# Kernel optimization log

Hardware: AMD Instinct MI355X
Metric: run time of the kernel (lower is better)

The kernel has to match this reference:

```python
import jax, jax.numpy as jnp
import numpy as np

B, S, IN_DIM, D_MODEL, H = 1, 4096, 512, 512, 8
DK = D_MODEL // H


def setup_inputs() -> dict:
    key = jax.random.key(0)
    ks = jax.random.split(key, 10)
    sc_in = 1.0 / np.sqrt(IN_DIM)
    sc_dm = 1.0 / np.sqrt(D_MODEL)
    return {
        "x": jax.random.normal(ks[0], (B, S, IN_DIM), dtype=jnp.float32),
        "mask": jax.random.randint(ks[1], (1, 1, S, S), 0, 2, dtype=jnp.int32),
        "wq_w": jax.random.uniform(ks[2], (D_MODEL, IN_DIM), jnp.float32, -sc_in, sc_in),
        "wq_b": jax.random.uniform(ks[3], (D_MODEL,), jnp.float32, -sc_in, sc_in),
        "wk_w": jax.random.uniform(ks[4], (D_MODEL, IN_DIM), jnp.float32, -sc_in, sc_in),
        "wk_b": jax.random.uniform(ks[5], (D_MODEL,), jnp.float32, -sc_in, sc_in),
        "wv_w": jax.random.uniform(ks[6], (D_MODEL, IN_DIM), jnp.float32, -sc_in, sc_in),
        "wv_b": jax.random.uniform(ks[7], (D_MODEL,), jnp.float32, -sc_in, sc_in),
        "dense_w": jax.random.uniform(ks[8], (D_MODEL, D_MODEL), jnp.float32, -sc_dm, sc_dm),
        "dense_b": jax.random.uniform(ks[9], (D_MODEL,), jnp.float32, -sc_dm, sc_dm),
    }


def _split_heads(t):
    # Faithful to original: raw view [B, S, D] -> [B, H, S, DK] (no transpose)
    return t.reshape(B, H, S, DK)


def reference(x, mask, wq_w, wq_b, wk_w, wk_b, wv_w, wv_b, dense_w, dense_b):
    q = _split_heads(x @ wq_w.T + wq_b)  # [B, H, S, DK]
    k = _split_heads(x @ wk_w.T + wk_b)
    v = _split_heads(x @ wv_w.T + wv_b)
    score = jnp.einsum("bhqd,bhkd->bhqk", q, k) / np.sqrt(DK).astype(np.float32)
    score = score + mask.astype(score.dtype) * (-1e9)
    attn = jax.nn.softmax(score, axis=-1)
    out = jnp.einsum("bhqk,bhkd->bhqd", attn, v)  # [B, H, S, DK]
    out = out.transpose(0, 2, 1, 3).reshape(B, S, D_MODEL)
    return out @ dense_w.T + dense_b
```

## Files before the change

kernel.cpp:

```cpp
#include <hip/hip_runtime.h>
#include <hip/hip_bf16.h>

#define S_LEN 4096
#define DM    512
#define NH    8
#define DK    64

typedef __attribute__((ext_vector_type(8))) __bf16 bf16x8;
typedef __attribute__((ext_vector_type(4))) float  f32x4;
typedef unsigned short u16;
typedef unsigned int   u32;
typedef unsigned long long u64;

#define SQ_SCALE (0.125f * 1.44269504f)
#define FMAX 12.0f

#define NPART 8
#define KSPAN 512

__device__ __forceinline__ u16 f2bf(float f) {
  union { float f; u32 i; } v; v.f = f;
  u32 r = v.i + 0x7fff + ((v.i >> 16) & 1);
  return (u16)(r >> 16);
}
__device__ __forceinline__ float bf2f(u16 u) {
  union { u32 i; float f; } v; v.i = ((u32)u) << 16; return v.f;
}

__global__ __launch_bounds__(256) void pack_mask(const int* __restrict__ mask,
                                                 u64* __restrict__ out) {
  int gid = blockIdx.x * 256 + threadIdx.x;
  u64 b = __ballot(mask[gid] != 0);
  if ((threadIdx.x & 63) == 0) out[gid >> 6] = b;
}

__global__ __launch_bounds__(256) void convert_all(
    const float* __restrict__ x, const float* __restrict__ wq,
    const float* __restrict__ wk, const float* __restrict__ wv,
    const float* __restrict__ dw,
    u16* __restrict__ xb, u16* __restrict__ wcat, u16* __restrict__ dwb) {
  int b = blockIdx.x;
  const float* src; u16* dst; size_t off;
  if      (b < 2048) { src = x;  dst = xb;   off = (size_t)b * 1024; }
  else if (b < 2304) { src = wq; dst = wcat; off = (size_t)(b - 2048) * 1024; }
  else if (b < 2560) { src = wk; dst = wcat + 262144; off = (size_t)(b - 2304) * 1024; }
  else if (b < 2816) { src = wv; dst = wcat + 524288; off = (size_t)(b - 2560) * 1024; }
  else               { src = dw; dst = dwb;  off = (size_t)(b - 2816) * 1024; }
  size_t i = off + (size_t)threadIdx.x * 4;
  float4 v = *reinterpret_cast<const float4*>(src + i);
  ushort4 o = make_ushort4(f2bf(v.x), f2bf(v.y), f2bf(v.z), f2bf(v.w));
  *reinterpret_cast<ushort4*>(dst + i) = o;
}

__global__ __launch_bounds__(256) void qkv_gemm(
    const u16* __restrict__ A, const u16* __restrict__ Wcat,
    const float* __restrict__ bq, const float* __restrict__ bk,
    const float* __restrict__ bv,
    u16* __restrict__ Qb, u16* __restrict__ Kb, u16* __restrict__ V4) {
  __shared__ u16 As[64 * 72];
  __shared__ u16 Ws[128 * 72];
  const int t = threadIdx.x;
  const int lane = t & 63, wv = t >> 6;
  const int m16 = lane & 15, quad = lane >> 4;
  const int n0g = blockIdx.x * 128, m0 = blockIdx.y * 64;
  const int seg = n0g >> 9;
  const int n0 = n0g & 511;
  const int mq = wv >> 1, nq = wv & 1;

  f32x4 acc[2][4];
#pragma unroll
  for (int i = 0; i < 2; i++)
#pragma unroll
    for (int j = 0; j < 4; j++) acc[i][j] = (f32x4)0.f;

  for (int k0 = 0; k0 < DM; k0 += 64) {
    __syncthreads();
#pragma unroll
    for (int c0 = 0; c0 < 2; c0++) {
      int c = t + c0 * 256;
      int row = c >> 3, col = (c & 7) * 8;
      *reinterpret_cast<uint4*>(&As[row * 72 + col]) =
          *reinterpret_cast<const uint4*>(&A[(size_t)(m0 + row) * DM + k0 + col]);
    }
#pragma unroll
    for (int c0 = 0; c0 < 4; c0++) {
      int c = t + c0 * 256;
      int row = c >> 3, col = (c & 7) * 8;
      *reinterpret_cast<uint4*>(&Ws[row * 72 + col]) =
          *reinterpret_cast<const uint4*>(&Wcat[(size_t)(n0g + row) * DM + k0 + col]);
    }
    __syncthreads();
#pragma unroll
    for (int kk = 0; kk < 64; kk += 32) {
      bf16x8 a0 = *reinterpret_cast<const bf16x8*>(&As[(mq * 32 + m16) * 72 + quad * 8 + kk]);
      bf16x8 a1 = *reinterpret_cast<const bf16x8*>(&As[(mq * 32 + 16 + m16) * 72 + quad * 8 + kk]);
#pragma unroll
      for (int ct = 0; ct < 4; ct++) {
        bf16x8 b = *reinterpret_cast<const bf16x8*>(&Ws[(nq * 64 + ct * 16 + m16) * 72 + quad * 8 + kk]);
        acc[0][ct] = __builtin_amdgcn_mfma_f32_16x16x32_bf16(a0, b, acc[0][ct], 0, 0, 0);
        acc[1][ct] = __builtin_amdgcn_mfma_f32_16x16x32_bf16(a1, b, acc[1][ct], 0, 0, 0);
      }
    }
  }

  const float* bias = (seg == 0) ? bq : (seg == 1) ? bk : bv;
  const float scale = (seg == 0) ? SQ_SCALE : 1.f;
  float bn[4];
#pragma unroll
  for (int ct = 0; ct < 4; ct++) bn[ct] = bias[n0 + nq * 64 + ct * 16 + m16];

  if (seg == 2) {
    __syncthreads();
    u16* T = Ws;
#pragma unroll
    for (int rt = 0; rt < 2; rt++)
#pragma unroll
      for (int ct = 0; ct < 4; ct++)
#pragma unroll
        for (int r = 0; r < 4; r++)
          T[(nq * 64 + ct * 16 + m16) * 72 + mq * 32 + rt * 16 + quad * 4 + r] =
              f2bf(acc[rt][ct][r] + bn[ct]);
    __syncthreads();
    const int h    = m0 >> 9;
    const int mp   = m0 & 511;
    const int cseg = n0 >> 7;
#pragma unroll
    for (int c0 = 0; c0 < 4; c0++) {
      int c = t + c0 * 256;
      int d  = c >> 4;
      int tl = (c >> 1) & 7;
      int cl = c & 1;
      uint4 v = *reinterpret_cast<const uint4*>(&T[(cl * 64 + d) * 72 + tl * 8]);
      *reinterpret_cast<uint4*>(
          &V4[(size_t)(h * 64 + d) * 4096 + ((mp >> 3) + tl) * 64 + cl * 32 + cseg * 8]) = v;
    }
  } else {
    u16* dst = (seg == 0) ? Qb : Kb;
#pragma unroll
    for (int rt = 0; rt < 2; rt++)
#pragma unroll
      for (int ct = 0; ct < 4; ct++) {
        int n = n0 + nq * 64 + ct * 16 + m16;
#pragma unroll
        for (int r = 0; r < 4; r++) {
          int m = m0 + mq * 32 + rt * 16 + quad * 4 + r;
          dst[(size_t)m * DM + n] = f2bf((acc[rt][ct][r] + bn[ct]) * scale);
        }
      }
  }
}

__global__ __launch_bounds__(256) void dense_gemm(
    const u16* __restrict__ A, const u16* __restrict__ W,
    const float* __restrict__ bias, float* __restrict__ Cout) {
  __shared__ u16 As[64 * 72];
  __shared__ u16 Ws[64 * 72];
  const int t = threadIdx.x;
  const int lane = t & 63, wv = t >> 6;
  const int m16 = lane & 15, quad = lane >> 4;
  const int n0 = blockIdx.x * 64, m0 = blockIdx.y * 64;

  f32x4 acc[4];
#pragma unroll
  for (int j = 0; j < 4; j++) acc[j] = (f32x4)0.f;

  for (int k0 = 0; k0 < DM; k0 += 64) {
    __syncthreads();
#pragma unroll
    for (int c0 = 0; c0 < 2; c0++) {
      int c = t + c0 * 256;
      int row = c >> 3, col = (c & 7) * 8;
      *reinterpret_cast<uint4*>(&As[row * 72 + col]) =
          *reinterpret_cast<const uint4*>(&A[(size_t)(m0 + row) * DM + k0 + col]);
      *reinterpret_cast<uint4*>(&Ws[row * 72 + col]) =
          *reinterpret_cast<const uint4*>(&W[(size_t)(n0 + row) * DM + k0 + col]);
    }
    __syncthreads();
#pragma unroll
    for (int kk = 0; kk < 64; kk += 32) {
      bf16x8 a = *reinterpret_cast<const bf16x8*>(&As[(wv * 16 + m16) * 72 + quad * 8 + kk]);
#pragma unroll
      for (int ct = 0; ct < 4; ct++) {
        bf16x8 b = *reinterpret_cast<const bf16x8*>(&Ws[(ct * 16 + m16) * 72 + quad * 8 + kk]);
        acc[ct] = __builtin_amdgcn_mfma_f32_16x16x32_bf16(a, b, acc[ct], 0, 0, 0);
      }
    }
  }

  float bn[4];
#pragma unroll
  for (int ct = 0; ct < 4; ct++) bn[ct] = bias[n0 + ct * 16 + m16];
#pragma unroll
  for (int ct = 0; ct < 4; ct++) {
    int n = n0 + ct * 16 + m16;
#pragma unroll
    for (int r = 0; r < 4; r++) {
      int m = m0 + wv * 16 + quad * 4 + r;
      Cout[(size_t)m * DM + n] = acc[ct][r] + bn[ct];
    }
  }
}

__device__ __forceinline__ void pack_p(const f32x4* s, u32 lo, u32 hi,
                                       uint4& o0, uint4& o1) {
  u32 pk[8];
#pragma unroll
  for (int ct = 0; ct < 4; ct++) {
    u32 w = (ct & 1) ? hi : lo;
    int b = ct >> 1;
    float p0 = __builtin_amdgcn_exp2f(((w >> b) & 1u)        ? -1e9f : s[ct][0]);
    float p1 = __builtin_amdgcn_exp2f(((w >> (b + 8)) & 1u)  ? -1e9f : s[ct][1]);
    float p2 = __builtin_amdgcn_exp2f(((w >> (b + 16)) & 1u) ? -1e9f : s[ct][2]);
    float p3 = __builtin_amdgcn_exp2f(((w >> (b + 24)) & 1u) ? -1e9f : s[ct][3]);
    pk[2 * ct]     = __builtin_amdgcn_perm(__float_as_uint(p1) + 0x8000u,
                                           __float_as_uint(p0) + 0x8000u, 0x07060302u);
    pk[2 * ct + 1] = __builtin_amdgcn_perm(__float_as_uint(p3) + 0x8000u,
                                           __float_as_uint(p2) + 0x8000u, 0x07060302u);
  }
  o0 = make_uint4(pk[0], pk[1], pk[2], pk[3]);
  o1 = make_uint4(pk[4], pk[5], pk[6], pk[7]);
}

__global__ __launch_bounds__(256, 4) void attn_mfma(
    const u16* __restrict__ Q, const u16* __restrict__ K,
    const u16* __restrict__ V4, const u64* __restrict__ mbits,
    u16* __restrict__ Op, float* __restrict__ Lp) {
  __shared__ u16 Ks[64 * 72];
  __shared__ u16 Vs[64 * 72];

  const int t = threadIdx.x;
  const int lane = t & 63, w4 = t >> 6;
  const int m16 = lane & 15, quad = lane >> 4;
  const int q0 = blockIdx.x * 128;
  const int h = blockIdx.y;
  const int g = blockIdx.z;
  const size_t hoff = (size_t)h * S_LEN * DK;
  const size_t kbase = hoff + (size_t)g * KSPAN * DK;

  const u16* qpA = Q + hoff + (size_t)(q0 + w4 * 32 + m16) * DK + quad * 8;
  bf16x8 qloA = *reinterpret_cast<const bf16x8*>(qpA);
  bf16x8 qhiA = *reinterpret_cast<const bf16x8*>(qpA + 32);
  bf16x8 qloB = *reinterpret_cast<const bf16x8*>(qpA + 16 * DK);
  bf16x8 qhiB = *reinterpret_cast<const bf16x8*>(qpA + 16 * DK + 32);

  union { u16 u[8]; bf16x8 v; } onesu;
#pragma unroll
  for (int j = 0; j < 8; j++) onesu.u[j] = 0x3F80;
  const bf16x8 ones = onesu.v;

  f32x4 accA[4], accB[4];
  f32x4 acc_lA = (f32x4)0.f, acc_lB = (f32x4)0.f;
#pragma unroll
  for (int dt = 0; dt < 4; dt++) { accA[dt] = (f32x4)0.f; accB[dt] = (f32x4)0.f; }

  for (int k0 = 0; k0 < KSPAN; k0 += 64) {
    const int kg = g * KSPAN + k0;
#pragma unroll
    for (int c0 = 0; c0 < 2; c0++) {
      int c = t + c0 * 256;
      int rg = c >> 3, cc = c & 7;
      int sr = ((rg & 1) << 5) | (((rg >> 5) & 1) << 4) | (((rg >> 2) & 1) << 3) |
               (((rg >> 1) & 1) << 2) | (((rg >> 4) & 1) << 1) | ((rg >> 3) & 1);
      *reinterpret_cast<uint4*>(&Ks[sr * 72 + cc * 8]) =
          *reinterpret_cast<const uint4*>(&K[kbase + (size_t)(k0 + rg) * DK + cc * 8]);
      *reinterpret_cast<uint4*>(&Vs[rg * 72 + cc * 8]) =
          *reinterpret_cast<const uint4*>(&V4[(size_t)(h * 64 + rg) * 4096 + kg + cc * 8]);
    }
    u64 mqA = mbits[(size_t)(q0 + w4 * 32 + m16) * 64 + (kg >> 6)] >> (2 * quad);
    u64 mqB = mbits[(size_t)(q0 + w4 * 32 + 16 + m16) * 64 + (kg >> 6)] >> (2 * quad);
    __syncthreads();

    f32x4 sA[4], sB[4];
#pragma unroll
    for (int ct = 0; ct < 4; ct++) { sA[ct] = (f32x4)(-FMAX); sB[ct] = (f32x4)(-FMAX); }
#pragma unroll
    for (int ct = 0; ct < 4; ct++) {
      bf16x8 klo = *reinterpret_cast<const bf16x8*>(&Ks[(ct * 16 + m16) * 72 + quad * 8]);
      bf16x8 khi = *reinterpret_cast<const bf16x8*>(&Ks[(ct * 16 + m16) * 72 + quad * 8 + 32]);
      sA[ct] = __builtin_amdgcn_mfma_f32_16x16x32_bf16(klo, qloA, sA[ct], 0, 0, 0);
      sA[ct] = __builtin_amdgcn_mfma_f32_16x16x32_bf16(khi, qhiA, sA[ct], 0, 0, 0);
      sB[ct] = __builtin_amdgcn_mfma_f32_16x16x32_bf16(klo, qloB, sB[ct], 0, 0, 0);
      sB[ct] = __builtin_amdgcn_mfma_f32_16x16x32_bf16(khi, qhiB, sB[ct], 0, 0, 0);
    }

    union { uint4 i; bf16x8 v; } pA0, pA1, pB0, pB1;
    pack_p(sA, (u32)mqA, (u32)(mqA >> 32), pA0.i, pA1.i);
    pack_p(sB, (u32)mqB, (u32)(mqB >> 32), pB0.i, pB1.i);

#pragma unroll
    for (int dt = 0; dt < 4; dt++) {
      bf16x8 vlo = *reinterpret_cast<const bf16x8*>(&Vs[(dt * 16 + m16) * 72 + quad * 8]);
      bf16x8 vhi = *reinterpret_cast<const bf16x8*>(&Vs[(dt * 16 + m16) * 72 + quad * 8 + 32]);
      accA[dt] = __builtin_amdgcn_mfma_f32_16x16x32_bf16(pA0.v, vlo, accA[dt], 0, 0, 0);
      accA[dt] = __builtin_amdgcn_mfma_f32_16x16x32_bf16(pA1.v, vhi, accA[dt], 0, 0, 0);
      accB[dt] = __builtin_amdgcn_mfma_f32_16x16x32_bf16(pB0.v, vlo, accB[dt], 0, 0, 0);
      accB[dt] = __builtin_amdgcn_mfma_f32_16x16x32_bf16(pB1.v, vhi, accB[dt], 0, 0, 0);
    }
    acc_lA = __builtin_amdgcn_mfma_f32_16x16x32_bf16(pA0.v, ones, acc_lA, 0, 0, 0);
    acc_lA = __builtin_amdgcn_mfma_f32_16x16x32_bf16(pA1.v, ones, acc_lA, 0, 0, 0);
    acc_lB = __builtin_amdgcn_mfma_f32_16x16x32_bf16(pB0.v, ones, acc_lB, 0, 0, 0);
    acc_lB = __builtin_amdgcn_mfma_f32_16x16x32_bf16(pB1.v, ones, acc_lB, 0, 0, 0);
    __syncthreads();
  }

  u16* Og = Op + (size_t)g * 2097152;
#pragma unroll
  for (int dt = 0; dt < 4; dt++)
#pragma unroll
    for (int r = 0; r < 4; r++) {
      Og[(size_t)(q0 + w4 * 32 + quad * 4 + r) * DM + h * DK + dt * 16 + m16] =
          f2bf(accA[dt][r]);
      Og[(size_t)(q0 + w4 * 32 + 16 + quad * 4 + r) * DM + h * DK + dt * 16 + m16] =
          f2bf(accB[dt][r]);
    }
  if (m16 == 0) {
#pragma unroll
    for (int r = 0; r < 4; r++) {
      Lp[g * 32768 + h * 4096 + q0 + w4 * 32 + quad * 4 + r] = acc_lA[r];
      Lp[g * 32768 + h * 4096 + q0 + w4 * 32 + 16 + quad * 4 + r] = acc_lB[r];
    }
  }
}

__global__ __launch_bounds__(256) void attn_merge(
    const u16* __restrict__ Op, const float* __restrict__ Lp,
    u16* __restrict__ Out) {
  int i8 = (blockIdx.x * 256 + threadIdx.x) * 8;
  int q = i8 >> 9;
  int h = (i8 >> 6) & 7;
  float l = 0.f;
#pragma unroll
  for (int part = 0; part < NPART; part++) l += Lp[part * 32768 + h * 4096 + q];
  float rl = 1.f / l;
  float o[8];
#pragma unroll
  for (int j = 0; j < 8; j++) o[j] = 0.f;
#pragma unroll
  for (int part = 0; part < NPART; part++) {
    ushort4 v0 = *reinterpret_cast<const ushort4*>(Op + (size_t)part * 2097152 + i8);
    ushort4 v1 = *reinterpret_cast<const ushort4*>(Op + (size_t)part * 2097152 + i8 + 4);
    o[0] += bf2f(v0.x); o[1] += bf2f(v0.y); o[2] += bf2f(v0.z); o[3] += bf2f(v0.w);
    o[4] += bf2f(v1.x); o[5] += bf2f(v1.y); o[6] += bf2f(v1.z); o[7] += bf2f(v1.w);
  }
  ushort4 o0 = make_ushort4(f2bf(o[0] * rl), f2bf(o[1] * rl),
                            f2bf(o[2] * rl), f2bf(o[3] * rl));
  ushort4 o1 = make_ushort4(f2bf(o[4] * rl), f2bf(o[5] * rl),
                            f2bf(o[6] * rl), f2bf(o[7] * rl));
  *reinterpret_cast<ushort4*>(Out + i8) = o0;
  *reinterpret_cast<ushort4*>(Out + i8 + 4) = o1;
}

extern "C" void kernel_launch(void* const* d_in, const int* in_sizes, int n_in,
                              void* d_out, int out_size, void* d_ws, size_t ws_size,
                              hipStream_t stream) {
  const float* x    = (const float*)d_in[0];
  const int*   mask = (const int*)d_in[1];
  const float* wq_w = (const float*)d_in[2];
  const float* wq_b = (const float*)d_in[3];
  const float* wk_w = (const float*)d_in[4];
  const float* wk_b = (const float*)d_in[5];
  const float* wv_w = (const float*)d_in[6];
  const float* wv_b = (const float*)d_in[7];
  const float* dw   = (const float*)d_in[8];
  const float* db   = (const float*)d_in[9];

  u16* xb    = (u16*)d_ws;
  u16* wcat  = xb    + 2097152;
  u16* dwb   = wcat  + 786432;
  u16* Qb    = dwb   + 262144;
  u16* Kb    = Qb    + 2097152;
  u16* V4    = Kb    + 2097152;
  u16* Opart = V4    + 2097152;
  u64* mb    = (u64*)(Opart + (size_t)NPART * 2097152);
  float* Lp  = (float*)(mb + 262144);

  pack_mask<<<(S_LEN * S_LEN) / 256, 256, 0, stream>>>(mask, mb);
  convert_all<<<3072, 256, 0, stream>>>(x, wq_w, wk_w, wv_w, dw, xb, wcat, dwb);

  qkv_gemm<<<dim3(12, 64), 256, 0, stream>>>(xb, wcat, wq_b, wk_b, wv_b,
                                             Qb, Kb, V4);

  attn_mfma<<<dim3(32, NH, NPART), 256, 0, stream>>>(Qb, Kb, V4, mb, Opart, Lp);
  attn_merge<<<1024, 256, 0, stream>>>(Opart, Lp, Qb);

  dense_gemm<<<dim3(8, 64), 256, 0, stream>>>(Qb, dwb, db, (float*)d_out);
}
```

Before: 233.8 us.

## Register-prefetch next K/V tile, fold mask into accumulator init, halve key partitions

The attention loop now loads the next 64-key K/V tile and mask words into registers while the current tile is computed, then stores them to LDS at the top of the next iteration. This hides global-load latency behind the MFMA work. The mask is applied by initialising the score accumulators to -1e9 or -FMAX before the QK MFMAs, which removes the per-element selects from the exp packing. The key span per block doubles and the partition count halves, so there are fewer blocks and less partial-result combining, but each block runs longer and grid parallelism drops.

```diff
diff --git a/kernel.cpp b/kernel.cpp
--- a/kernel.cpp
+++ b/kernel.cpp
@@ -15,8 +15,8 @@
 #define SQ_SCALE (0.125f * 1.44269504f)
 #define FMAX 12.0f
 
-#define NPART 8
-#define KSPAN 512
+#define NPART 4
+#define KSPAN 1024
 
 __device__ __forceinline__ u16 f2bf(float f) {
   union { float f; u32 i; } v; v.f = f;
@@ -201,17 +201,14 @@
   }
 }
 
-__device__ __forceinline__ void pack_p(const f32x4* s, u32 lo, u32 hi,
-                                       uint4& o0, uint4& o1) {
+__device__ __forceinline__ void pack_p(const f32x4* s, uint4& o0, uint4& o1) {
   u32 pk[8];
 #pragma unroll
   for (int ct = 0; ct < 4; ct++) {
-    u32 w = (ct & 1) ? hi : lo;
-    int b = ct >> 1;
-    float p0 = __builtin_amdgcn_exp2f(((w >> b) & 1u)        ? -1e9f : s[ct][0]);
-    float p1 = __builtin_amdgcn_exp2f(((w >> (b + 8)) & 1u)  ? -1e9f : s[ct][1]);
-    float p2 = __builtin_amdgcn_exp2f(((w >> (b + 16)) & 1u) ? -1e9f : s[ct][2]);
-    float p3 = __builtin_amdgcn_exp2f(((w >> (b + 24)) & 1u) ? -1e9f : s[ct][3]);
+    float p0 = __builtin_amdgcn_exp2f(s[ct][0]);
+    float p1 = __builtin_amdgcn_exp2f(s[ct][1]);
+    float p2 = __builtin_amdgcn_exp2f(s[ct][2]);
+    float p3 = __builtin_amdgcn_exp2f(s[ct][3]);
     pk[2 * ct]     = __builtin_amdgcn_perm(__float_as_uint(p1) + 0x8000u,
                                            __float_as_uint(p0) + 0x8000u, 0x07060302u);
     pk[2 * ct + 1] = __builtin_amdgcn_perm(__float_as_uint(p3) + 0x8000u,
@@ -248,31 +245,65 @@
   for (int j = 0; j < 8; j++) onesu.u[j] = 0x3F80;
   const bf16x8 ones = onesu.v;
 
+  const int rg0 = t >> 3,          cc = t & 7;
+  const int rg1 = (t + 256) >> 3;
+  auto sigma = [](int rg) {
+    return ((rg & 1) << 5) | (((rg >> 5) & 1) << 4) | (((rg >> 2) & 1) << 3) |
+           (((rg >> 1) & 1) << 2) | (((rg >> 4) & 1) << 1) | ((rg >> 3) & 1);
+  };
+  const int sr0 = sigma(rg0), sr1 = sigma(rg1);
+  const u16* kp0 = &K[kbase + (size_t)rg0 * DK + cc * 8];
+  const u16* kp1 = &K[kbase + (size_t)rg1 * DK + cc * 8];
+  const u16* vp0 = &V4[(size_t)(h * 64 + rg0) * 4096 + g * KSPAN + cc * 8];
+  const u16* vp1 = &V4[(size_t)(h * 64 + rg1) * 4096 + g * KSPAN + cc * 8];
+  const u64* mpA = &mbits[(size_t)(q0 + w4 * 32 + m16) * 64 + ((g * KSPAN) >> 6)];
+  const u64* mpB = mpA + (size_t)16 * 64;
+
+  uint4 rk0 = *reinterpret_cast<const uint4*>(kp0);
+  uint4 rk1 = *reinterpret_cast<const uint4*>(kp1);
+  uint4 rv0 = *reinterpret_cast<const uint4*>(vp0);
+  uint4 rv1 = *reinterpret_cast<const uint4*>(vp1);
+  u64 rmA = *mpA, rmB = *mpB;
+
   f32x4 accA[4], accB[4];
   f32x4 acc_lA = (f32x4)0.f, acc_lB = (f32x4)0.f;
 #pragma unroll
   for (int dt = 0; dt < 4; dt++) { accA[dt] = (f32x4)0.f; accB[dt] = (f32x4)0.f; }
 
   for (int k0 = 0; k0 < KSPAN; k0 += 64) {
-    const int kg = g * KSPAN + k0;
-#pragma unroll
-    for (int c0 = 0; c0 < 2; c0++) {
-      int c = t + c0 * 256;
-      int rg = c >> 3, cc = c & 7;
-      int sr = ((rg & 1) << 5) | (((rg >> 5) & 1) << 4) | (((rg >> 2) & 1) << 3) |
-               (((rg >> 1) & 1) << 2) | (((rg >> 4) & 1) << 1) | ((rg >> 3) & 1);
-      *reinterpret_cast<uint4*>(&Ks[sr * 72 + cc * 8]) =
-          *reinterpret_cast<const uint4*>(&K[kbase + (size_t)(k0 + rg) * DK + cc * 8]);
-      *reinterpret_cast<uint4*>(&Vs[rg * 72 + cc * 8]) =
-          *reinterpret_cast<const uint4*>(&V4[(size_t)(h * 64 + rg) * 4096 + kg + cc * 8]);
-    }
-    u64 mqA = mbits[(size_t)(q0 + w4 * 32 + m16) * 64 + (kg >> 6)] >> (2 * quad);
-    u64 mqB = mbits[(size_t)(q0 + w4 * 32 + 16 + m16) * 64 + (kg >> 6)] >> (2 * quad);
+    __syncthreads();
+    *reinterpret_cast<uint4*>(&Ks[sr0 * 72 + cc * 8]) = rk0;
+    *reinterpret_cast<uint4*>(&Ks[sr1 * 72 + cc * 8]) = rk1;
+    *reinterpret_cast<uint4*>(&Vs[rg0 * 72 + cc * 8]) = rv0;
+    *reinterpret_cast<uint4*>(&Vs[rg1 * 72 + cc * 8]) = rv1;
+    u64 mA = rmA >> (2 * quad);
+    u64 mB = rmB >> (2 * quad);
+    if (k0 + 64 < KSPAN) {
+      kp0 += 64 * DK; kp1 += 64 * DK; vp0 += 64; vp1 += 64;
+      rk0 = *reinterpret_cast<const uint4*>(kp0);
+      rk1 = *reinterpret_cast<const uint4*>(kp1);
+      rv0 = *reinterpret_cast<const uint4*>(vp0);
+      rv1 = *reinterpret_cast<const uint4*>(vp1);
+      rmA = mpA[(k0 >> 6) + 1];
+      rmB = mpB[(k0 >> 6) + 1];
+    }
     __syncthreads();
 
     f32x4 sA[4], sB[4];
-#pragma unroll
-    for (int ct = 0; ct < 4; ct++) { sA[ct] = (f32x4)(-FMAX); sB[ct] = (f32x4)(-FMAX); }
+    u32 loA = (u32)mA, hiA = (u32)(mA >> 32);
+    u32 loB = (u32)mB, hiB = (u32)(mB >> 32);
+#pragma unroll
+    for (int ct = 0; ct < 4; ct++) {
+      u32 wA = (ct & 1) ? hiA : loA;
+      u32 wB = (ct & 1) ? hiB : loB;
+      int b = ct >> 1;
+#pragma unroll
+      for (int r = 0; r < 4; r++) {
+        sA[ct][r] = ((wA >> (b + 8 * r)) & 1u) ? -1e9f : -FMAX;
+        sB[ct][r] = ((wB >> (b + 8 * r)) & 1u) ? -1e9f : -FMAX;
+      }
+    }
+
 #pragma unroll
     for (int ct = 0; ct < 4; ct++) {
       bf16x8 klo = *reinterpret_cast<const bf16x8*>(&Ks[(ct * 16 + m16) * 72 + quad * 8]);
@@ -284,8 +315,8 @@
     }
 
     union { uint4 i; bf16x8 v; } pA0, pA1, pB0, pB1;
-    pack_p(sA, (u32)mqA, (u32)(mqA >> 32), pA0.i, pA1.i);
-    pack_p(sB, (u32)mqB, (u32)(mqB >> 32), pB0.i, pB1.i);
+    pack_p(sA, pA0.i, pA1.i);
+    pack_p(sB, pB0.i, pB1.i);
 
 #pragma unroll
     for (int dt = 0; dt < 4; dt++) {
@@ -300,7 +331,6 @@
     acc_lA = __builtin_amdgcn_mfma_f32_16x16x32_bf16(pA1.v, ones, acc_lA, 0, 0, 0);
     acc_lB = __builtin_amdgcn_mfma_f32_16x16x32_bf16(pB0.v, ones, acc_lB, 0, 0, 0);
     acc_lB = __builtin_amdgcn_mfma_f32_16x16x32_bf16(pB1.v, ones, acc_lB, 0, 0, 0);
-    __syncthreads();
   }
 
   u16* Og = Op + (size_t)g * 2097152;
```

Result: slower. 252.2 us (+7.9%).

## Load K/V fragments directly from global memory, drop LDS and barriers, remap grid

Applied to the files above, without the earlier changes.

The attention kernel no longer stages K and V tiles through shared memory with __syncthreads; each lane reads its MFMA operand fragments straight from global memory, with the K row permutation folded into precomputed per-lane pointers. The split-K factor goes from 8 partitions of 512 keys to 4 partitions of 1024, and the grid is flattened to 1024 blocks with a custom index mapping so that the blocks sharing a q-tile land near each other. This removes LDS traffic and barrier stalls, but the four waves in a block each reload the same K/V data from L1/L2 and get fewer but longer blocks. The merge kernel still launches 1024 blocks over partials, so it relies on the unseen merge code using NPART.

```diff
diff --git a/kernel.cpp b/kernel.cpp
--- a/kernel.cpp
+++ b/kernel.cpp
@@ -15,8 +15,8 @@
 #define SQ_SCALE (0.125f * 1.44269504f)
 #define FMAX 12.0f
 
-#define NPART 8
-#define KSPAN 512
+#define NPART 4
+#define KSPAN 1024
 
 __device__ __forceinline__ u16 f2bf(float f) {
   union { float f; u32 i; } v; v.f = f;
@@ -225,15 +225,14 @@
     const u16* __restrict__ Q, const u16* __restrict__ K,
     const u16* __restrict__ V4, const u64* __restrict__ mbits,
     u16* __restrict__ Op, float* __restrict__ Lp) {
-  __shared__ u16 Ks[64 * 72];
-  __shared__ u16 Vs[64 * 72];
-
   const int t = threadIdx.x;
   const int lane = t & 63, w4 = t >> 6;
   const int m16 = lane & 15, quad = lane >> 4;
-  const int q0 = blockIdx.x * 128;
-  const int h = blockIdx.y;
-  const int g = blockIdx.z;
+  const int lin = blockIdx.x;
+  const int q0 = ((lin >> 3) & 31) * 128;
+  const int hg = ((lin >> 8) << 3) | (lin & 7);
+  const int h = hg & 7;
+  const int g = hg >> 3;
   const size_t hoff = (size_t)h * S_LEN * DK;
   const size_t kbase = hoff + (size_t)g * KSPAN * DK;
 
@@ -243,6 +242,14 @@
   bf16x8 qloB = *reinterpret_cast<const bf16x8*>(qpA + 16 * DK);
   bf16x8 qhiB = *reinterpret_cast<const bf16x8*>(qpA + 16 * DK + 32);
 
+  const u16* kct[4];
+#pragma unroll
+  for (int ct = 0; ct < 4; ct++) {
+    int row = ((ct & 1) << 5) | (((m16 >> 1) & 1) << 4) | ((m16 & 1) << 3) |
+              (((m16 >> 3) & 1) << 2) | (((m16 >> 2) & 1) << 1) | (ct >> 1);
+    kct[ct] = K + kbase + (size_t)row * DK + quad * 8;
+  }
+
   union { u16 u[8]; bf16x8 v; } onesu;
 #pragma unroll
   for (int j = 0; j < 8; j++) onesu.u[j] = 0x3F80;
@@ -253,30 +260,23 @@
 #pragma unroll
   for (int dt = 0; dt < 4; dt++) { accA[dt] = (f32x4)0.f; accB[dt] = (f32x4)0.f; }
 
+  const u16* vt0 = V4 + (size_t)(h * 64 + m16) * 4096 + g * KSPAN + quad * 8;
+  const u64* mpA = &mbits[(size_t)(q0 + w4 * 32 + m16) * 64 + ((g * KSPAN) >> 6)];
+  const u64* mpB = mpA + (size_t)16 * 64;
+
+#pragma unroll 1
   for (int k0 = 0; k0 < KSPAN; k0 += 64) {
-    const int kg = g * KSPAN + k0;
-#pragma unroll
-    for (int c0 = 0; c0 < 2; c0++) {
-      int c = t + c0 * 256;
-      int rg = c >> 3, cc = c & 7;
-      int sr = ((rg & 1) << 5) | (((rg >> 5) & 1) << 4) | (((rg >> 2) & 1) << 3) |
-               (((rg >> 1) & 1) << 2) | (((rg >> 4) & 1) << 1) | ((rg >> 3) & 1);
-      *reinterpret_cast<uint4*>(&Ks[sr * 72 + cc * 8]) =
-          *reinterpret_cast<const uint4*>(&K[kbase + (size_t)(k0 + rg) * DK + cc * 8]);
-      *reinterpret_cast<uint4*>(&Vs[rg * 72 + cc * 8]) =
-          *reinterpret_cast<const uint4*>(&V4[(size_t)(h * 64 + rg) * 4096 + kg + cc * 8]);
-    }
-    u64 mqA = mbits[(size_t)(q0 + w4 * 32 + m16) * 64 + (kg >> 6)] >> (2 * quad);
-    u64 mqB = mbits[(size_t)(q0 + w4 * 32 + 16 + m16) * 64 + (kg >> 6)] >> (2 * quad);
-    __syncthreads();
+    u64 mqA = mpA[k0 >> 6] >> (2 * quad);
+    u64 mqB = mpB[k0 >> 6] >> (2 * quad);
 
     f32x4 sA[4], sB[4];
 #pragma unroll
     for (int ct = 0; ct < 4; ct++) { sA[ct] = (f32x4)(-FMAX); sB[ct] = (f32x4)(-FMAX); }
+    const size_t koff = (size_t)k0 * DK;
 #pragma unroll
     for (int ct = 0; ct < 4; ct++) {
-      bf16x8 klo = *reinterpret_cast<const bf16x8*>(&Ks[(ct * 16 + m16) * 72 + quad * 8]);
-      bf16x8 khi = *reinterpret_cast<const bf16x8*>(&Ks[(ct * 16 + m16) * 72 + quad * 8 + 32]);
+      bf16x8 klo = *reinterpret_cast<const bf16x8*>(kct[ct] + koff);
+      bf16x8 khi = *reinterpret_cast<const bf16x8*>(kct[ct] + koff + 32);
       sA[ct] = __builtin_amdgcn_mfma_f32_16x16x32_bf16(klo, qloA, sA[ct], 0, 0, 0);
       sA[ct] = __builtin_amdgcn_mfma_f32_16x16x32_bf16(khi, qhiA, sA[ct], 0, 0, 0);
       sB[ct] = __builtin_amdgcn_mfma_f32_16x16x32_bf16(klo, qloB, sB[ct], 0, 0, 0);
@@ -287,10 +287,11 @@
     pack_p(sA, (u32)mqA, (u32)(mqA >> 32), pA0.i, pA1.i);
     pack_p(sB, (u32)mqB, (u32)(mqB >> 32), pB0.i, pB1.i);
 
+    const u16* vt = vt0 + k0;
 #pragma unroll
     for (int dt = 0; dt < 4; dt++) {
-      bf16x8 vlo = *reinterpret_cast<const bf16x8*>(&Vs[(dt * 16 + m16) * 72 + quad * 8]);
-      bf16x8 vhi = *reinterpret_cast<const bf16x8*>(&Vs[(dt * 16 + m16) * 72 + quad * 8 + 32]);
+      bf16x8 vlo = *reinterpret_cast<const bf16x8*>(vt + dt * 16 * 4096);
+      bf16x8 vhi = *reinterpret_cast<const bf16x8*>(vt + dt * 16 * 4096 + 32);
       accA[dt] = __builtin_amdgcn_mfma_f32_16x16x32_bf16(pA0.v, vlo, accA[dt], 0, 0, 0);
       accA[dt] = __builtin_amdgcn_mfma_f32_16x16x32_bf16(pA1.v, vhi, accA[dt], 0, 0, 0);
       accB[dt] = __builtin_amdgcn_mfma_f32_16x16x32_bf16(pB0.v, vlo, accB[dt], 0, 0, 0);
@@ -300,7 +301,6 @@
     acc_lA = __builtin_amdgcn_mfma_f32_16x16x32_bf16(pA1.v, ones, acc_lA, 0, 0, 0);
     acc_lB = __builtin_amdgcn_mfma_f32_16x16x32_bf16(pB0.v, ones, acc_lB, 0, 0, 0);
     acc_lB = __builtin_amdgcn_mfma_f32_16x16x32_bf16(pB1.v, ones, acc_lB, 0, 0, 0);
-    __syncthreads();
   }
 
   u16* Og = Op + (size_t)g * 2097152;
@@ -380,7 +380,7 @@
   qkv_gemm<<<dim3(12, 64), 256, 0, stream>>>(xb, wcat, wq_b, wk_b, wv_b,
                                              Qb, Kb, V4);
 
-  attn_mfma<<<dim3(32, NH, NPART), 256, 0, stream>>>(Qb, Kb, V4, mb, Opart, Lp);
+  attn_mfma<<<1024, 256, 0, stream>>>(Qb, Kb, V4, mb, Opart, Lp);
   attn_merge<<<1024, 256, 0, stream>>>(Opart, Lp, Qb);
 
   dense_gemm<<<dim3(8, 64), 256, 0, stream>>>(Qb, dwb, db, (float*)d_out);
```

Result: slower. 295.5 us (+26.4%).
